# Performance work log

Measured on AMD Instinct MI355X. Metric: run time of the kernel, lower is better.

The kernel has to match this reference:

```python
import jax, jax.numpy as jnp
import numpy as np
from jax import lax

EMB, H1, H2 = 100, 128, 64  # embedding_dim, hidden_dim, hidden_dim//2
B, T = 1024, 512


def _uniform(key, shape, scale):
    return jax.random.uniform(key, shape, jnp.float32, -scale, scale)


def setup_inputs() -> dict:
    key = jax.random.key(0)
    ks = jax.random.split(key, 16)
    s1 = 1.0 / np.sqrt(H1)
    s2 = 1.0 / np.sqrt(H2)
    return {
        "X": jax.random.normal(ks[0], (B, T, EMB), jnp.float32),
        # PyTorch LSTM weights, gate order (i, f, g, o)
        "W1_ih": _uniform(ks[1], (4 * H1, EMB), s1),
        "W1_hh": _uniform(ks[2], (4 * H1, H1), s1),
        "b1_ih": _uniform(ks[3], (4 * H1,), s1),
        "b1_hh": _uniform(ks[4], (4 * H1,), s1),
        "W2_ih": _uniform(ks[5], (4 * H2, H1), s2),
        "W2_hh": _uniform(ks[6], (4 * H2, H2), s2),
        "b2_ih": _uniform(ks[7], (4 * H2,), s2),
        "b2_hh": _uniform(ks[8], (4 * H2,), s2),
        "fc1_w": _uniform(ks[9], (32, H2), 1.0 / np.sqrt(H2)),
        "fc1_b": _uniform(ks[10], (32,), 1.0 / np.sqrt(H2)),
        "fc2_w": _uniform(ks[11], (1, 32), 1.0 / np.sqrt(32)),
        "fc2_b": _uniform(ks[12], (1,), 1.0 / np.sqrt(32)),
    }


def _lstm(x, W_ih, W_hh, b_ih, b_hh):
    # x: [B, T, D]; returns (all hidden states [B, T, H], final h [B, H])
    Bb = x.shape[0]
    H = W_hh.shape[1]
    # Batch the input projection across all timesteps (one big GEMM).
    xw = jnp.einsum('btd,gd->tbg', x, W_ih) + (b_ih + b_hh)  # [T, B, 4H]

    def step(carry, xt):
        h, c = carry
        gates = xt + h @ W_hh.T  # [B, 4H]
        i, f, g, o = jnp.split(gates, 4, axis=-1)
        c = jax.nn.sigmoid(f) * c + jax.nn.sigmoid(i) * jnp.tanh(g)
        h = jax.nn.sigmoid(o) * jnp.tanh(c)
        return (h, c), h

    h0 = jnp.zeros((Bb, H), x.dtype)
    (h_n, _), hs = lax.scan(step, (h0, h0), xw)
    return jnp.swapaxes(hs, 0, 1), h_n


def reference(X, W1_ih, W1_hh, b1_ih, b1_hh,
              W2_ih, W2_hh, b2_ih, b2_hh,
              fc1_w, fc1_b, fc2_w, fc2_b):
    hs1, _ = _lstm(X, W1_ih, W1_hh, b1_ih, b1_hh)        # [B, T, 128]
    # dropout is identity at inference
    _, h_n = _lstm(hs1, W2_ih, W2_hh, b2_ih, b2_hh)      # [B, 64]
    x = jax.nn.relu(h_n @ fc1_w.T + fc1_b)               # [B, 32]
    x = x @ fc2_w.T + fc2_b                              # [B, 1]
    return jax.nn.sigmoid(x)[:, 0]                       # [B]
```

## Files before the change

kernel.cpp:

```cpp
#include <hip/hip_runtime.h>
#include <hip/hip_fp16.h>

typedef _Float16 half8 __attribute__((ext_vector_type(8)));
typedef _Float16 half4 __attribute__((ext_vector_type(4)));
typedef float floatx4 __attribute__((ext_vector_type(4)));

#define TT 512
#define EE 100
#define NBATCH 16
#define NBLK 64
#define WS_NEED ((size_t)NBLK * TT * 2048 * sizeof(_Float16))

__device__ __forceinline__ float sigm(float x) {
    return __builtin_amdgcn_rcpf(1.0f + __expf(-x));
}
__device__ __forceinline__ float tanh_(float x) {
    return __builtin_amdgcn_rcpf(1.0f + __expf(-2.0f * x)) * 2.0f - 1.0f;
}
__device__ __forceinline__ half4 cvt4(float4 v) {
    half4 h; h[0] = (_Float16)v.x; h[1] = (_Float16)v.y; h[2] = (_Float16)v.z; h[3] = (_Float16)v.w;
    return h;
}

extern "C" __global__ void __launch_bounds__(256)
xfrag_prep(const float* __restrict__ X, _Float16* __restrict__ xw)
{
    const int bt  = blockIdx.x;
    const int blk = bt >> 9;
    const int t   = bt & (TT - 1);
    const int tid = threadIdx.x;
    const int c   = tid >> 4, m = tid & 15;
    const int k0  = 8 * c;
    half8 v;
#pragma unroll
    for (int j = 0; j < 8; ++j) v[j] = (_Float16)0.0f;
    const float* p = X + ((size_t)(blk * 16 + m) * TT + t) * EE + k0;
    if (k0 + 8 <= EE) {
        float4 lo = *(const float4*)p;
        float4 hi = *(const float4*)(p + 4);
        v[0] = (_Float16)lo.x; v[1] = (_Float16)lo.y; v[2] = (_Float16)lo.z; v[3] = (_Float16)lo.w;
        v[4] = (_Float16)hi.x; v[5] = (_Float16)hi.y; v[6] = (_Float16)hi.z; v[7] = (_Float16)hi.w;
    } else if (k0 < EE) {
        float4 lo = *(const float4*)p;
        v[0] = (_Float16)lo.x; v[1] = (_Float16)lo.y; v[2] = (_Float16)lo.z; v[3] = (_Float16)lo.w;
        v[4] = (_Float16)1.0f;
    }
    *(half8*)&xw[(size_t)bt * 2048 + c * 128 + m * 8] = v;
}

template<int USE_WS>
__global__ void __launch_bounds__(512, 1)
lstm_mfma3(const float* __restrict__ X, const _Float16* __restrict__ xw,
           const float* __restrict__ W1ih, const float* __restrict__ W1hh,
           const float* __restrict__ b1i,  const float* __restrict__ b1h,
           const float* __restrict__ W2ih, const float* __restrict__ W2hh,
           const float* __restrict__ b2i,  const float* __restrict__ b2h,
           const float* __restrict__ fc1w, const float* __restrict__ fc1b,
           const float* __restrict__ fc2w, const float* __restrict__ fc2b,
           float* __restrict__ out)
{
    const int tid  = threadIdx.x;
    const int w    = tid >> 6;
    const int lane = tid & 63;
    const int q    = lane >> 4;
    const int m    = lane & 15;
    const int b0   = blockIdx.x * NBATCH;
    const int gh   = w >> 2;
    const int p2   = w & 3;

    __shared__ __align__(16) _Float16 h1b[2][4][4][16][8];
    __shared__ __align__(16) _Float16 h2b[2][2][4][16][8];
    __shared__ __align__(16) _Float16 xb [2][4][4][16][8];
    __shared__ __align__(16) _Float16 gob[2][16][68];
    __shared__ float fca[NBATCH][32];

    {
        _Float16* p = &h1b[0][0][0][0][0];
        for (int i = tid; i < 2 * 2048; i += 512) p[i] = (_Float16)0.0f;
        p = &h2b[0][0][0][0][0];
        for (int i = tid; i < 2 * 1024; i += 512) p[i] = (_Float16)0.0f;
        if (!USE_WS) {
            p = &xb[0][0][0][0][0];
            for (int i = tid; i < 2 * 2048; i += 512) p[i] = (_Float16)0.0f;
        }
    }

    half8 w1ihf[4][4], w1hhf[4][4], w2ihf[2][4], w2hhf[2][2];
    floatx4 bias2v[2];
#pragma unroll
    for (int g = 0; g < 4; ++g) {
        const int r = g * 128 + 16 * w + m;
        const float bias = b1i[r] + b1h[r];
#pragma unroll
        for (int s = 0; s < 4; ++s) {
            half8 f;
#pragma unroll
            for (int j = 0; j < 8; ++j) {
                const int k = 32 * s + 8 * q + j;
                float v = 0.0f;
                if (k < EE) v = W1ih[r * EE + k];
                else if (k == EE) v = bias;
                f[j] = (_Float16)v;
            }
            w1ihf[g][s] = f;
        }
#pragma unroll
        for (int s = 0; s < 4; ++s) {
            half8 f;
#pragma unroll
            for (int j = 0; j < 8; ++j) f[j] = (_Float16)W1hh[r * 128 + 32 * s + 8 * q + j];
            w1hhf[g][s] = f;
        }
    }
#pragma unroll
    for (int tau = 0; tau < 2; ++tau) {
        const int g = 2 * gh + tau;
        const int r = g * 64 + 16 * p2 + m;
#pragma unroll
        for (int s = 0; s < 4; ++s) {
            half8 f;
#pragma unroll
            for (int j = 0; j < 8; ++j) f[j] = (_Float16)W2ih[r * 128 + 32 * s + 8 * q + j];
            w2ihf[tau][s] = f;
        }
#pragma unroll
        for (int s = 0; s < 2; ++s) {
            half8 f;
#pragma unroll
            for (int j = 0; j < 8; ++j) f[j] = (_Float16)W2hh[r * 64 + 32 * s + 8 * q + j];
            w2hhf[tau][s] = f;
        }
#pragma unroll
        for (int reg = 0; reg < 4; ++reg) {
            const int rr = g * 64 + 16 * p2 + 4 * q + reg;
            bias2v[tau][reg] = b2i[rr] + b2h[rr];
        }
    }

    const _Float16* xwb = xw + (size_t)blockIdx.x * TT * 2048;
    const int foff = q * 128 + m * 8;
    half8 xcur[4], xnxt[4];

    int gaddr = 0, laddr = 0;
    bool xval = false;
    float4 xr = {0.f, 0.f, 0.f, 0.f};
    if (!USE_WS) {
        xval = tid < 400;
        const int f = xval ? tid : 0;
        const int n = f / 25, pp = f - 25 * n, e0 = 4 * pp;
        gaddr = (b0 + n) * (TT * EE) + e0;
        const int s = e0 >> 5, qr = (e0 >> 3) & 3, j0 = e0 & 7;
        laddr = ((s * 4 + qr) * 16 + n) * 8 + j0;
    }

    __syncthreads();
    if (USE_WS) {
#pragma unroll
        for (int s = 0; s < 4; ++s) xcur[s] = *(const half8*)&xwb[s * 512 + foff];
    } else {
        if (tid < 32) { const int bf = tid >> 4, mm = tid & 15; xb[bf][3][0][mm][4] = (_Float16)1.0f; }
        if (xval) {
            *(half4*)&(((_Float16*)xb)[laddr]) = cvt4(*(const float4*)&X[gaddr]);
            xr = *(const float4*)&X[gaddr + EE];
        }
    }
    __syncthreads();

    floatx4 c1 = {0.f, 0.f, 0.f, 0.f};
    floatx4 c2 = {0.f, 0.f, 0.f, 0.f};
    const int vv = 2 * w + (q >> 1);
    const int v2 = 2 * p2 + (q >> 1);
    const int jj = 4 * (q & 1);

#pragma unroll 1
    for (int t = 0; t < TT; ++t) {
        const int cur = t & 1, nxt = cur ^ 1;

        if (USE_WS) {
            const int tn = (t + 1 < TT) ? (t + 1) : (TT - 1);
            const _Float16* xp = xwb + tn * 2048 + foff;
#pragma unroll
            for (int s = 0; s < 4; ++s) xnxt[s] = *(const half8*)(xp + s * 512);
        }

        floatx4 a1[4];
#pragma unroll
        for (int g = 0; g < 4; ++g) a1[g] = (floatx4){0.f, 0.f, 0.f, 0.f};
        {
            const _Float16* xc = ((const _Float16*)xb) + cur * 2048 + foff;
#pragma unroll
            for (int s = 0; s < 4; ++s) {
                half8 bx = USE_WS ? xcur[s] : *(const half8*)(xc + s * 512);
#pragma unroll
                for (int g = 0; g < 4; ++g)
                    a1[g] = __builtin_amdgcn_mfma_f32_16x16x32_f16(w1ihf[g][s], bx, a1[g], 0, 0, 0);
            }
            const _Float16* hp = ((const _Float16*)h1b) + nxt * 2048 + foff;
#pragma unroll
            for (int s = 0; s < 4; ++s) {
                half8 bh = *(const half8*)(hp + s * 512);
#pragma unroll
                for (int g = 0; g < 4; ++g)
                    a1[g] = __builtin_amdgcn_mfma_f32_16x16x32_f16(w1hhf[g][s], bh, a1[g], 0, 0, 0);
            }
        }

        if (!USE_WS) {
            if (xval) *(half4*)&(((_Float16*)xb)[nxt * 2048 + laddr]) = cvt4(xr);
            const int tn2 = (t + 2 < TT) ? (t + 2) : (TT - 1);
            if (xval) xr = *(const float4*)&X[gaddr + tn2 * EE];
        }

        {
            half4 hv;
#pragma unroll
            for (int r = 0; r < 4; ++r) {
                const float iv = sigm(a1[0][r]);
                const float fv = sigm(a1[1][r]);
                const float gv = tanh_(a1[2][r]);
                const float ov = sigm(a1[3][r]);
                const float c  = fv * c1[r] + iv * gv;
                c1[r] = c;
                hv[r] = (_Float16)(ov * tanh_(c));
            }
            *(half4*)&h1b[cur][vv >> 2][vv & 3][m][jj] = hv;
        }
        __syncthreads();

        floatx4 a2[2] = { bias2v[0], bias2v[1] };
        {
            const _Float16* hc = ((const _Float16*)h1b) + cur * 2048 + foff;
#pragma unroll
            for (int s = 0; s < 4; ++s) {
                half8 bh = *(const half8*)(hc + s * 512);
                a2[0] = __builtin_amdgcn_mfma_f32_16x16x32_f16(w2ihf[0][s], bh, a2[0], 0, 0, 0);
                a2[1] = __builtin_amdgcn_mfma_f32_16x16x32_f16(w2ihf[1][s], bh, a2[1], 0, 0, 0);
            }
            const _Float16* h2p = ((const _Float16*)h2b) + nxt * 1024 + foff;
#pragma unroll
            for (int s = 0; s < 2; ++s) {
                half8 b2v = *(const half8*)(h2p + s * 512);
                a2[0] = __builtin_amdgcn_mfma_f32_16x16x32_f16(w2hhf[0][s], b2v, a2[0], 0, 0, 0);
                a2[1] = __builtin_amdgcn_mfma_f32_16x16x32_f16(w2hhf[1][s], b2v, a2[1], 0, 0, 0);
            }
        }

        if (gh == 1) {
            half4 tg, so;
#pragma unroll
            for (int r = 0; r < 4; ++r) {
                tg[r] = (_Float16)tanh_(a2[0][r]);
                so[r] = (_Float16)sigm(a2[1][r]);
            }
            *(half4*)&gob[0][m][16 * p2 + 4 * q] = tg;
            *(half4*)&gob[1][m][16 * p2 + 4 * q] = so;
        }
        if (USE_WS) {
#pragma unroll
            for (int s = 0; s < 4; ++s) xcur[s] = xnxt[s];
        }
        __syncthreads();

        if (gh == 0) {
            half4 tg = *(const half4*)&gob[0][m][16 * p2 + 4 * q];
            half4 so = *(const half4*)&gob[1][m][16 * p2 + 4 * q];
            half4 hv;
#pragma unroll
            for (int r = 0; r < 4; ++r) {
                const float c = sigm(a2[1][r]) * c2[r] + sigm(a2[0][r]) * (float)tg[r];
                c2[r] = c;
                hv[r] = (_Float16)((float)so[r] * tanh_(c));
            }
            *(half4*)&h2b[cur][v2 >> 2][v2 & 3][m][jj] = hv;
        }
    }
    __syncthreads();

    {
        const int nb = tid >> 5, o = tid & 31;
        float s = fc1b[o];
#pragma unroll
        for (int k = 0; k < 64; ++k)
            s += fc1w[o * 64 + k] * (float)h2b[1][k >> 5][(k >> 3) & 3][nb][k & 7];
        fca[nb][o] = fmaxf(s, 0.0f);
    }
    __syncthreads();
    if (tid < NBATCH) {
        float s = fc2b[0];
#pragma unroll
        for (int k = 0; k < 32; ++k) s += fc2w[k] * fca[tid][k];
        out[b0 + tid] = sigm(s);
    }
}

extern "C" void kernel_launch(void* const* d_in, const int* in_sizes, int n_in,
                              void* d_out, int out_size, void* d_ws, size_t ws_size,
                              hipStream_t stream) {
    const float* X    = (const float*)d_in[0];
    const float* W1ih = (const float*)d_in[1];
    const float* W1hh = (const float*)d_in[2];
    const float* b1i  = (const float*)d_in[3];
    const float* b1h  = (const float*)d_in[4];
    const float* W2ih = (const float*)d_in[5];
    const float* W2hh = (const float*)d_in[6];
    const float* b2i  = (const float*)d_in[7];
    const float* b2h  = (const float*)d_in[8];
    const float* fc1w = (const float*)d_in[9];
    const float* fc1b = (const float*)d_in[10];
    const float* fc2w = (const float*)d_in[11];
    const float* fc2b = (const float*)d_in[12];
    _Float16* xw = (_Float16*)d_ws;

    if (ws_size >= WS_NEED) {
        hipLaunchKernelGGL(xfrag_prep, dim3(NBLK * TT), dim3(256), 0, stream, X, xw);
        hipLaunchKernelGGL(lstm_mfma3<1>, dim3(NBLK), dim3(512), 0, stream,
                           X, xw, W1ih, W1hh, b1i, b1h, W2ih, W2hh, b2i, b2h,
                           fc1w, fc1b, fc2w, fc2b, (float*)d_out);
    } else {
        hipLaunchKernelGGL(lstm_mfma3<0>, dim3(NBLK), dim3(512), 0, stream,
                           X, xw, W1ih, W1hh, b1i, b1h, W2ih, W2hh, b2i, b2h,
                           fc1w, fc1b, fc2w, fc2b, (float*)d_out);
    }
}
```

Baseline: 1.103 ms.

## Interleave LSTM2 gate rows per wave, drop gate exchange barrier, prefetch x via LDS DMA

Layer-2 weight rows are permuted so each lane holds all four gates (i,f,g,o) of one hidden unit. The cell update can then finish in registers, which removes the shared gob exchange buffer and one __syncthreads per timestep. The input projection for step t+1 moves off the recurrent critical path by computing it after the layer-2 MFMAs. The x fragments are now prefetched two steps ahead straight into LDS with global_load_lds instead of through registers. The trade-offs are more complex indexing, scalar fp16 stores into h2, and reliance on the async LDS load finishing before the next barrier.

```diff
diff --git a/kernel.cpp b/kernel.cpp
--- a/kernel.cpp
+++ b/kernel.cpp
@@ -10,6 +10,11 @@
 #define NBATCH 16
 #define NBLK 64
 #define WS_NEED ((size_t)NBLK * TT * 2048 * sizeof(_Float16))
+
+typedef const __attribute__((address_space(1))) void gvoid_t;
+typedef __attribute__((address_space(3))) void lvoid_t;
+
+#define MFMA16 __builtin_amdgcn_mfma_f32_16x16x32_f16
 
 __device__ __forceinline__ float sigm(float x) {
     return __builtin_amdgcn_rcpf(1.0f + __expf(-x));
@@ -50,7 +55,7 @@
 
 template<int USE_WS>
 __global__ void __launch_bounds__(512, 1)
-lstm_mfma3(const float* __restrict__ X, const _Float16* __restrict__ xw,
+lstm_mfma4(const float* __restrict__ X, const _Float16* __restrict__ xw,
            const float* __restrict__ W1ih, const float* __restrict__ W1hh,
            const float* __restrict__ b1i,  const float* __restrict__ b1h,
            const float* __restrict__ W2ih, const float* __restrict__ W2hh,
@@ -65,23 +70,23 @@
     const int q    = lane >> 4;
     const int m    = lane & 15;
     const int b0   = blockIdx.x * NBATCH;
-    const int gh   = w >> 2;
-    const int p2   = w & 3;
 
     __shared__ __align__(16) _Float16 h1b[2][4][4][16][8];
     __shared__ __align__(16) _Float16 h2b[2][2][4][16][8];
     __shared__ __align__(16) _Float16 xb [2][4][4][16][8];
-    __shared__ __align__(16) _Float16 gob[2][16][68];
     __shared__ float fca[NBATCH][32];
 
-    {
-        _Float16* p = &h1b[0][0][0][0][0];
-        for (int i = tid; i < 2 * 2048; i += 512) p[i] = (_Float16)0.0f;
-        p = &h2b[0][0][0][0][0];
-        for (int i = tid; i < 2 * 1024; i += 512) p[i] = (_Float16)0.0f;
-        if (!USE_WS) {
-            p = &xb[0][0][0][0][0];
-            for (int i = tid; i < 2 * 2048; i += 512) p[i] = (_Float16)0.0f;
+    _Float16* const h1f = &h1b[0][0][0][0][0];
+    _Float16* const h2f = &h2b[0][0][0][0][0];
+    _Float16* const xbf = &xb [0][0][0][0][0];
+
+    for (int i = tid; i < 2 * 2048; i += 512) h1f[i] = (_Float16)0.0f;
+    for (int i = tid; i < 2 * 1024; i += 512) h2f[i] = (_Float16)0.0f;
+    if (!USE_WS) {
+        for (int i = tid; i < 2 * 2048; i += 512) {
+            const int k = i & 2047;
+            xbf[i] = (k >= 1536 && k < 1664 && (k & 7) == 4) ? (_Float16)1.0f
+                                                             : (_Float16)0.0f;
         }
     }
 
@@ -114,32 +119,29 @@
     }
 #pragma unroll
     for (int tau = 0; tau < 2; ++tau) {
-        const int g = 2 * gh + tau;
-        const int r = g * 64 + 16 * p2 + m;
+        const int rr = (m & 3) * 64 + 8 * w + 4 * tau + (m >> 2);
 #pragma unroll
         for (int s = 0; s < 4; ++s) {
             half8 f;
 #pragma unroll
-            for (int j = 0; j < 8; ++j) f[j] = (_Float16)W2ih[r * 128 + 32 * s + 8 * q + j];
+            for (int j = 0; j < 8; ++j) f[j] = (_Float16)W2ih[rr * 128 + 32 * s + 8 * q + j];
             w2ihf[tau][s] = f;
         }
 #pragma unroll
         for (int s = 0; s < 2; ++s) {
             half8 f;
 #pragma unroll
-            for (int j = 0; j < 8; ++j) f[j] = (_Float16)W2hh[r * 64 + 32 * s + 8 * q + j];
+            for (int j = 0; j < 8; ++j) f[j] = (_Float16)W2hh[rr * 64 + 32 * s + 8 * q + j];
             w2hhf[tau][s] = f;
         }
-#pragma unroll
-        for (int reg = 0; reg < 4; ++reg) {
-            const int rr = g * 64 + 16 * p2 + 4 * q + reg;
-            bias2v[tau][reg] = b2i[rr] + b2h[rr];
-        }
+        const int uu = 8 * w + 4 * tau + q;
+#pragma unroll
+        for (int reg = 0; reg < 4; ++reg)
+            bias2v[tau][reg] = b2i[reg * 64 + uu] + b2h[reg * 64 + uu];
     }
 
     const _Float16* xwb = xw + (size_t)blockIdx.x * TT * 2048;
     const int foff = q * 128 + m * 8;
-    half8 xcur[4], xnxt[4];
 
     int gaddr = 0, laddr = 0;
     bool xval = false;
@@ -154,71 +156,61 @@
     }
 
     __syncthreads();
+
     if (USE_WS) {
-#pragma unroll
-        for (int s = 0; s < 4; ++s) xcur[s] = *(const half8*)&xwb[s * 512 + foff];
-    } else {
-        if (tid < 32) { const int bf = tid >> 4, mm = tid & 15; xb[bf][3][0][mm][4] = (_Float16)1.0f; }
-        if (xval) {
-            *(half4*)&(((_Float16*)xb)[laddr]) = cvt4(*(const float4*)&X[gaddr]);
-            xr = *(const float4*)&X[gaddr + EE];
-        }
+        if (w < 4) {
+            __builtin_amdgcn_global_load_lds((gvoid_t*)(xwb + 0 * 2048 + w * 512 + lane * 8),
+                                             (lvoid_t*)(xbf + 0 * 2048 + w * 512), 16, 0, 0);
+            __builtin_amdgcn_global_load_lds((gvoid_t*)(xwb + 1 * 2048 + w * 512 + lane * 8),
+                                             (lvoid_t*)(xbf + 1 * 2048 + w * 512), 16, 0, 0);
+        }
+    } else if (xval) {
+        *(half4*)&xbf[0 * 2048 + laddr] = cvt4(*(const float4*)&X[gaddr + 0 * EE]);
+        *(half4*)&xbf[1 * 2048 + laddr] = cvt4(*(const float4*)&X[gaddr + 1 * EE]);
+        xr = *(const float4*)&X[gaddr + 2 * EE];
     }
     __syncthreads();
 
+    floatx4 a1x[4];
+#pragma unroll
+    for (int g = 0; g < 4; ++g) a1x[g] = (floatx4){0.f, 0.f, 0.f, 0.f};
+    {
+        const _Float16* xc = xbf + 0 * 2048 + foff;
+#pragma unroll
+        for (int s = 0; s < 4; ++s) {
+            half8 bx = *(const half8*)(xc + s * 512);
+#pragma unroll
+            for (int g = 0; g < 4; ++g) a1x[g] = MFMA16(w1ihf[g][s], bx, a1x[g], 0, 0, 0);
+        }
+    }
+
     floatx4 c1 = {0.f, 0.f, 0.f, 0.f};
-    floatx4 c2 = {0.f, 0.f, 0.f, 0.f};
+    float c2[2] = {0.f, 0.f};
     const int vv = 2 * w + (q >> 1);
-    const int v2 = 2 * p2 + (q >> 1);
     const int jj = 4 * (q & 1);
 
 #pragma unroll 1
     for (int t = 0; t < TT; ++t) {
         const int cur = t & 1, nxt = cur ^ 1;
 
-        if (USE_WS) {
-            const int tn = (t + 1 < TT) ? (t + 1) : (TT - 1);
-            const _Float16* xp = xwb + tn * 2048 + foff;
-#pragma unroll
-            for (int s = 0; s < 4; ++s) xnxt[s] = *(const half8*)(xp + s * 512);
-        }
-
-        floatx4 a1[4];
-#pragma unroll
-        for (int g = 0; g < 4; ++g) a1[g] = (floatx4){0.f, 0.f, 0.f, 0.f};
         {
-            const _Float16* xc = ((const _Float16*)xb) + cur * 2048 + foff;
-#pragma unroll
-            for (int s = 0; s < 4; ++s) {
-                half8 bx = USE_WS ? xcur[s] : *(const half8*)(xc + s * 512);
-#pragma unroll
-                for (int g = 0; g < 4; ++g)
-                    a1[g] = __builtin_amdgcn_mfma_f32_16x16x32_f16(w1ihf[g][s], bx, a1[g], 0, 0, 0);
-            }
-            const _Float16* hp = ((const _Float16*)h1b) + nxt * 2048 + foff;
+            const _Float16* hp = h1f + nxt * 2048 + foff;
 #pragma unroll
             for (int s = 0; s < 4; ++s) {
                 half8 bh = *(const half8*)(hp + s * 512);
 #pragma unroll
                 for (int g = 0; g < 4; ++g)
-                    a1[g] = __builtin_amdgcn_mfma_f32_16x16x32_f16(w1hhf[g][s], bh, a1[g], 0, 0, 0);
-            }
-        }
-
-        if (!USE_WS) {
-            if (xval) *(half4*)&(((_Float16*)xb)[nxt * 2048 + laddr]) = cvt4(xr);
-            const int tn2 = (t + 2 < TT) ? (t + 2) : (TT - 1);
-            if (xval) xr = *(const float4*)&X[gaddr + tn2 * EE];
-        }
-
+                    a1x[g] = MFMA16(w1hhf[g][s], bh, a1x[g], 0, 0, 0);
+            }
+        }
         {
             half4 hv;
 #pragma unroll
             for (int r = 0; r < 4; ++r) {
-                const float iv = sigm(a1[0][r]);
-                const float fv = sigm(a1[1][r]);
-                const float gv = tanh_(a1[2][r]);
-                const float ov = sigm(a1[3][r]);
+                const float iv = sigm(a1x[0][r]);
+                const float fv = sigm(a1x[1][r]);
+                const float gv = tanh_(a1x[2][r]);
+                const float ov = sigm(a1x[3][r]);
                 const float c  = fv * c1[r] + iv * gv;
                 c1[r] = c;
                 hv[r] = (_Float16)(ov * tanh_(c));
@@ -227,51 +219,60 @@
         }
         __syncthreads();
 
+        if (USE_WS) {
+            if (w < 4) {
+                const int tn = (t + 2 < TT) ? (t + 2) : (TT - 1);
+                __builtin_amdgcn_global_load_lds((gvoid_t*)(xwb + (size_t)tn * 2048 + w * 512 + lane * 8),
+                                                 (lvoid_t*)(xbf + cur * 2048 + w * 512), 16, 0, 0);
+            }
+        } else if (xval) {
+            *(half4*)&xbf[cur * 2048 + laddr] = cvt4(xr);
+            const int tn = (t + 3 < TT) ? (t + 3) : (TT - 1);
+            xr = *(const float4*)&X[gaddr + tn * EE];
+        }
+
         floatx4 a2[2] = { bias2v[0], bias2v[1] };
         {
-            const _Float16* hc = ((const _Float16*)h1b) + cur * 2048 + foff;
+            const _Float16* hc = h1f + cur * 2048 + foff;
 #pragma unroll
             for (int s = 0; s < 4; ++s) {
                 half8 bh = *(const half8*)(hc + s * 512);
-                a2[0] = __builtin_amdgcn_mfma_f32_16x16x32_f16(w2ihf[0][s], bh, a2[0], 0, 0, 0);
-                a2[1] = __builtin_amdgcn_mfma_f32_16x16x32_f16(w2ihf[1][s], bh, a2[1], 0, 0, 0);
-            }
-            const _Float16* h2p = ((const _Float16*)h2b) + nxt * 1024 + foff;
+                a2[0] = MFMA16(w2ihf[0][s], bh, a2[0], 0, 0, 0);
+                a2[1] = MFMA16(w2ihf[1][s], bh, a2[1], 0, 0, 0);
+            }
+            const _Float16* h2p = h2f + nxt * 1024 + foff;
 #pragma unroll
             for (int s = 0; s < 2; ++s) {
                 half8 b2v = *(const half8*)(h2p + s * 512);
-                a2[0] = __builtin_amdgcn_mfma_f32_16x16x32_f16(w2hhf[0][s], b2v, a2[0], 0, 0, 0);
-                a2[1] = __builtin_amdgcn_mfma_f32_16x16x32_f16(w2hhf[1][s], b2v, a2[1], 0, 0, 0);
-            }
-        }
-
-        if (gh == 1) {
-            half4 tg, so;
-#pragma unroll
-            for (int r = 0; r < 4; ++r) {
-                tg[r] = (_Float16)tanh_(a2[0][r]);
-                so[r] = (_Float16)sigm(a2[1][r]);
-            }
-            *(half4*)&gob[0][m][16 * p2 + 4 * q] = tg;
-            *(half4*)&gob[1][m][16 * p2 + 4 * q] = so;
-        }
-        if (USE_WS) {
-#pragma unroll
-            for (int s = 0; s < 4; ++s) xcur[s] = xnxt[s];
-        }
-        __syncthreads();
-
-        if (gh == 0) {
-            half4 tg = *(const half4*)&gob[0][m][16 * p2 + 4 * q];
-            half4 so = *(const half4*)&gob[1][m][16 * p2 + 4 * q];
-            half4 hv;
-#pragma unroll
-            for (int r = 0; r < 4; ++r) {
-                const float c = sigm(a2[1][r]) * c2[r] + sigm(a2[0][r]) * (float)tg[r];
-                c2[r] = c;
-                hv[r] = (_Float16)((float)so[r] * tanh_(c));
-            }
-            *(half4*)&h2b[cur][v2 >> 2][v2 & 3][m][jj] = hv;
+                a2[0] = MFMA16(w2hhf[0][s], b2v, a2[0], 0, 0, 0);
+                a2[1] = MFMA16(w2hhf[1][s], b2v, a2[1], 0, 0, 0);
+            }
+        }
+
+        {
+            const _Float16* xc = xbf + nxt * 2048 + foff;
+#pragma unroll
+            for (int g = 0; g < 4; ++g) a1x[g] = (floatx4){0.f, 0.f, 0.f, 0.f};
+#pragma unroll
+            for (int s = 0; s < 4; ++s) {
+                half8 bx = *(const half8*)(xc + s * 512);
+#pragma unroll
+                for (int g = 0; g < 4; ++g)
+                    a1x[g] = MFMA16(w1ihf[g][s], bx, a1x[g], 0, 0, 0);
+            }
+        }
+
+#pragma unroll
+        for (int tau = 0; tau < 2; ++tau) {
+            const float iv = sigm(a2[tau][0]);
+            const float fv = sigm(a2[tau][1]);
+            const float gv = tanh_(a2[tau][2]);
+            const float ov = sigm(a2[tau][3]);
+            const float c  = fv * c2[tau] + iv * gv;
+            c2[tau] = c;
+            const int u = 8 * w + 4 * tau + q;
+            h2f[cur * 1024 + (u >> 5) * 512 + ((u >> 3) & 3) * 128 + m * 8 + (u & 7)]
+                = (_Float16)(ov * tanh_(c));
         }
     }
     __syncthreads();
@@ -313,11 +314,11 @@
 
     if (ws_size >= WS_NEED) {
         hipLaunchKernelGGL(xfrag_prep, dim3(NBLK * TT), dim3(256), 0, stream, X, xw);
-        hipLaunchKernelGGL(lstm_mfma3<1>, dim3(NBLK), dim3(512), 0, stream,
+        hipLaunchKernelGGL(lstm_mfma4<1>, dim3(NBLK), dim3(512), 0, stream,
                            X, xw, W1ih, W1hh, b1i, b1h, W2ih, W2hh, b2i, b2h,
                            fc1w, fc1b, fc2w, fc2b, (float*)d_out);
     } else {
-        hipLaunchKernelGGL(lstm_mfma3<0>, dim3(NBLK), dim3(512), 0, stream,
+        hipLaunchKernelGGL(lstm_mfma4<0>, dim3(NBLK), dim3(512), 0, stream,
                            X, xw, W1ih, W1hh, b1i, b1h, W2ih, W2hh, b2i, b2h,
                            fc1w, fc1b, fc2w, fc2b, (float*)d_out);
     }
```

Result: slower. 1.128 ms (+2.2%).
